# Kernel tuning notes

Measured on AMD Instinct MI355X. Metric: run time of the kernel, lower is better.

## Reference

```python
import jax, jax.numpy as jnp
import numpy as np

H = 32       # total query heads
HK = 8       # kv heads (GQA)
D = 128      # head_dim = hidden // H
HIDDEN = 4096
THETA = 10000.0


def setup_inputs() -> dict:
    key = jax.random.key(0)
    k1, k2, k3 = jax.random.split(key, 3)
    B, S = 2, 2048
    positions = jnp.arange(S, dtype=jnp.int32)
    hidden_states = jax.random.normal(k1, (B, S, HIDDEN), dtype=jnp.float32)
    w_qkv = jax.random.normal(k2, (HIDDEN, (H + 2 * HK) * D), dtype=jnp.float32) * 0.02
    w_o = jax.random.normal(k3, (H * D, HIDDEN), dtype=jnp.float32) * 0.02
    return {"positions": positions, "hidden_states": hidden_states,
            "w_qkv": w_qkv, "w_o": w_o}


def _rope(x, cos, sin):
    # neox-style rotary: split halves, rotate
    x1, x2 = jnp.split(x, 2, axis=-1)
    return jnp.concatenate([x1 * cos - x2 * sin, x2 * cos + x1 * sin], axis=-1)


def reference(positions, hidden_states, w_qkv, w_o):
    B, S, _ = hidden_states.shape
    qkv = hidden_states @ w_qkv                        # [B,S,(H+2HK)*D]
    q, k, v = jnp.split(qkv, [H * D, H * D + HK * D], axis=-1)
    q = q.reshape(B, S, H, D)
    k = k.reshape(B, S, HK, D)
    v = v.reshape(B, S, HK, D)

    inv_freq = 1.0 / (THETA ** (jnp.arange(0, D, 2, dtype=jnp.float32) / D))
    freqs = positions.astype(jnp.float32)[:, None] * inv_freq[None, :]  # [S,D/2]
    cos = jnp.cos(freqs)[None, :, None, :]
    sin = jnp.sin(freqs)[None, :, None, :]
    q = _rope(q, cos, sin)
    k = _rope(k, cos, sin)

    G = H // HK  # query heads per kv head
    qg = q.reshape(B, S, HK, G, D)
    scores = jnp.einsum('bqhgd,bkhd->bhgqk', qg, k) * (D ** -0.5)
    causal = jnp.tril(jnp.ones((S, S), dtype=bool))
    scores = jnp.where(causal[None, None, None], scores, jnp.float32(-1e30))
    probs = jax.nn.softmax(scores, axis=-1)
    out = jnp.einsum('bhgqk,bkhd->bqhgd', probs, v).reshape(B, S, H * D)
    return out @ w_o
```

## Files before the change

kernel.cpp:

```cpp
#include <hip/hip_runtime.h>

typedef unsigned short ushort_t;
typedef __attribute__((ext_vector_type(8))) short short8;
typedef __attribute__((ext_vector_type(4))) unsigned short ushort4_t;
typedef __attribute__((ext_vector_type(4))) float f32x4;

#define NH 32
#define NHK 8
#define HD 128
#define HID 4096
#define NB 2
#define SEQ 2048
#define NQKV ((NH + 2 * NHK) * HD)

static __device__ inline ushort_t f2bu(float x) {
  unsigned u = __builtin_bit_cast(unsigned, x);
  unsigned r = (u + 0x7FFFu + ((u >> 16) & 1u)) >> 16;
  return (ushort_t)r;
}

typedef __attribute__((address_space(1))) void gvoid;
typedef __attribute__((address_space(3))) void lvoid;
static __device__ inline void gld16(const void* g, void* l) {
  __builtin_amdgcn_global_load_lds((gvoid*)g, (lvoid*)l, 16, 0, 0);
}

__global__ void rope_tab_k(const int* __restrict__ positions, float* __restrict__ tab) {
  int i = blockIdx.x * 256 + threadIdx.x;
  int s = i >> 6, d = i & 63;
  float pos = (float)positions[s];
  float f = pos * exp2f(-0.20762050593046014f * (float)d);
  tab[2 * i] = cosf(f);
  tab[2 * i + 1] = sinf(f);
}

__global__ void h2b_k(const float* __restrict__ in, ushort_t* __restrict__ out) {
  long i = ((long)blockIdx.x * 256 + threadIdx.x) * 8;
  f32x4 a = *(const f32x4*)&in[i];
  f32x4 b = *(const f32x4*)&in[i + 4];
  ushort4_t ya, yb;
#pragma unroll
  for (int u = 0; u < 4; ++u) { ya[u] = f2bu(a[u]); yb[u] = f2bu(b[u]); }
  *(ushort4_t*)&out[i] = ya;
  *(ushort4_t*)&out[i + 4] = yb;
}

__global__ void wt_k(const float* __restrict__ in, ushort_t* __restrict__ out,
                     int K, int N) {
  __shared__ ushort_t T[64][72];
  int n0 = blockIdx.x * 64, k0 = blockIdx.y * 64;
  int t = threadIdx.x;
  int kr = t >> 4, nc = (t & 15) * 4;
#pragma unroll
  for (int p = 0; p < 4; ++p) {
    int k = kr + p * 16;
    f32x4 x = *(const f32x4*)&in[(long)(k0 + k) * N + n0 + nc];
    ushort4_t y;
#pragma unroll
    for (int u = 0; u < 4; ++u) y[u] = f2bu(x[u]);
    *(ushort4_t*)&T[k][nc] = y;
  }
  __syncthreads();
  int n = t >> 2, kc = (t & 3) * 16;
  ushort_t tmp[16];
#pragma unroll
  for (int j = 0; j < 16; ++j) tmp[j] = T[kc + j][n];
  *(short8*)&out[(long)(n0 + n) * K + k0 + kc] = *(short8*)&tmp[0];
  *(short8*)&out[(long)(n0 + n) * K + k0 + kc + 8] = *(short8*)&tmp[8];
}

template <int MODE>
__global__ __attribute__((amdgpu_flat_work_group_size(256, 256),
                          amdgpu_waves_per_eu(2, 2)))
void gemm_bt(const ushort_t* __restrict__ A,
             const ushort_t* __restrict__ Bt,
             float* __restrict__ C,
             const float* __restrict__ tab,
             ushort_t* __restrict__ Qo,
             ushort_t* __restrict__ Ko,
             ushort_t* __restrict__ Vo,
             int M, int N, int K) {
  __shared__ ushort_t As[128 * 32];
  __shared__ ushort_t Bs[128 * 32];
  int m0 = blockIdx.y * 128, n0 = blockIdx.x * 128;
  int tid = threadIdx.x;
  int lane = tid & 63, wave = tid >> 6;
  int wm = wave * 32;
  int l15 = lane & 15, quad = lane >> 4;
  f32x4 acc[2][8];
#pragma unroll
  for (int i = 0; i < 2; ++i)
#pragma unroll
    for (int j = 0; j < 8; ++j) acc[i][j] = (f32x4){0.f, 0.f, 0.f, 0.f};

  int iw = wave * 2;
  for (int k0 = 0; k0 < K; k0 += 32) {
    __syncthreads();
#pragma unroll
    for (int ii = 0; ii < 2; ++ii) {
      int i = iw + ii;
      int row = i * 16 + (lane >> 2);
      int gk = ((lane & 3) ^ ((row >> 1) & 3)) * 8;
      gld16(&A[(long)(m0 + row) * K + k0 + gk], &As[i * 512]);
      gld16(&Bt[(long)(n0 + row) * K + k0 + gk], &Bs[i * 512]);
    }
    __syncthreads();
    short8 af[2], bfr[8];
#pragma unroll
    for (int i = 0; i < 2; ++i) {
      int r = wm + i * 16 + l15;
      af[i] = *(short8*)&As[r * 32 + ((quad ^ ((r >> 1) & 3)) << 3)];
    }
#pragma unroll
    for (int j = 0; j < 8; ++j) {
      int r = j * 16 + l15;
      bfr[j] = *(short8*)&Bs[r * 32 + ((quad ^ ((r >> 1) & 3)) << 3)];
    }
#pragma unroll
    for (int i = 0; i < 2; ++i)
#pragma unroll
      for (int j = 0; j < 8; ++j)
        acc[i][j] = __builtin_amdgcn_mfma_f32_16x16x32_bf16(af[i], bfr[j], acc[i][j], 0, 0, 0);
  }

  if (MODE == 0) {
#pragma unroll
    for (int i = 0; i < 2; ++i)
#pragma unroll
      for (int j = 0; j < 8; ++j)
#pragma unroll
        for (int r = 0; r < 4; ++r) {
          int row = m0 + wm + i * 16 + quad * 4 + r;
          int col = n0 + j * 16 + l15;
          C[(long)row * N + col] = acc[i][j][r];
        }
  } else {
    int head = n0 >> 7;
    const float2* tb = (const float2*)tab;
    if (head < NH + NHK) {
      bool isq = head < NH;
      ushort_t* dst = isq ? (Qo + (long)head * SEQ * HD)
                          : (Ko + (long)(head - NH) * SEQ * HD);
      float sc = isq ? 0.08838834764831845f : 1.0f;
#pragma unroll
      for (int i = 0; i < 2; ++i)
#pragma unroll
        for (int r = 0; r < 4; ++r) {
          int s = m0 + wm + i * 16 + quad * 4 + r;
#pragma unroll
          for (int j = 0; j < 4; ++j) {
            int d = j * 16 + l15;
            float2 cs = tb[s * 64 + d];
            float x1 = acc[i][j][r], x2 = acc[i][j + 4][r];
            dst[(long)s * HD + d] = f2bu((x1 * cs.x - x2 * cs.y) * sc);
            dst[(long)s * HD + d + 64] = f2bu((x2 * cs.x + x1 * cs.y) * sc);
          }
        }
    } else {
      int hk = head - NH - NHK;
      ushort_t* dst = Vo + (long)hk * HD * SEQ;
#pragma unroll
      for (int i = 0; i < 2; ++i)
#pragma unroll
        for (int j = 0; j < 8; ++j)
#pragma unroll
          for (int r = 0; r < 4; ++r) {
            int s = m0 + wm + i * 16 + quad * 4 + r;
            int d = j * 16 + l15;
            dst[(long)d * SEQ + s] = f2bu(acc[i][j][r]);
          }
    }
  }
}

template <int MODE, typename TA>
__global__ __attribute__((amdgpu_flat_work_group_size(256, 256),
                          amdgpu_waves_per_eu(2, 2)))
void gemm_kn(const TA* __restrict__ A,
             const float* __restrict__ B,
             float* __restrict__ C,
             const float* __restrict__ tab,
             ushort_t* __restrict__ Qo,
             ushort_t* __restrict__ Ko,
             ushort_t* __restrict__ Vo,
             int M, int N, int K) {
  __shared__ ushort_t As[128][40];
  __shared__ ushort_t Bs[128 * 32];
  int m0 = blockIdx.y * 128, n0 = blockIdx.x * 128;
  int tid = threadIdx.x;
  int lane = tid & 63, wave = tid >> 6;
  int wm = wave * 32;
  int l15 = lane & 15, quad = lane >> 4;
  f32x4 acc[2][8];
#pragma unroll
  for (int i = 0; i < 2; ++i)
#pragma unroll
    for (int j = 0; j < 8; ++j) acc[i][j] = (f32x4){0.f, 0.f, 0.f, 0.f};

  for (int k0 = 0; k0 < K; k0 += 32) {
    __syncthreads();
    if constexpr (sizeof(TA) == 2) {
#pragma unroll
      for (int it = 0; it < 2; ++it) {
        int v = tid + it * 256;
        int row = v >> 2, kc = (v & 3) * 8;
        *(short8*)&As[row][kc] =
            *(const short8*)&A[(long)(m0 + row) * K + k0 + kc];
      }
    } else {
#pragma unroll
      for (int it = 0; it < 4; ++it) {
        int v = tid + it * 256;
        int row = v >> 3, kc = (v & 7) * 4;
        f32x4 x = *(const f32x4*)&A[(long)(m0 + row) * K + k0 + kc];
        ushort4_t y;
#pragma unroll
        for (int u = 0; u < 4; ++u) y[u] = f2bu(x[u]);
        *(ushort4_t*)&As[row][kc] = y;
      }
    }
#pragma unroll
    for (int it = 0; it < 4; ++it) {
      int v = tid + it * 256;
      int kr = v >> 5, nc = (v & 31) * 4;
      f32x4 x = *(const f32x4*)&B[(long)(k0 + kr) * N + n0 + nc];
      int kg = (kr >> 3) << 3, ke = kr & 7;
#pragma unroll
      for (int u = 0; u < 4; ++u) {
        int n = nc + u;
        Bs[n * 32 + ((kg ^ (((n >> 2) & 3) << 3))) + ke] = f2bu(x[u]);
      }
    }
    __syncthreads();
    short8 af[2], bfr[8];
#pragma unroll
    for (int i = 0; i < 2; ++i) af[i] = *(short8*)&As[wm + i * 16 + l15][quad * 8];
#pragma unroll
    for (int j = 0; j < 8; ++j) {
      int n = j * 16 + l15;
      bfr[j] = *(short8*)&Bs[n * 32 + ((quad ^ ((n >> 2) & 3)) << 3)];
    }
#pragma unroll
    for (int i = 0; i < 2; ++i)
#pragma unroll
      for (int j = 0; j < 8; ++j)
        acc[i][j] = __builtin_amdgcn_mfma_f32_16x16x32_bf16(af[i], bfr[j], acc[i][j], 0, 0, 0);
  }

  if (MODE == 0) {
#pragma unroll
    for (int i = 0; i < 2; ++i)
#pragma unroll
      for (int j = 0; j < 8; ++j)
#pragma unroll
        for (int r = 0; r < 4; ++r) {
          int row = m0 + wm + i * 16 + quad * 4 + r;
          int col = n0 + j * 16 + l15;
          C[(long)row * N + col] = acc[i][j][r];
        }
  } else {
    int head = n0 >> 7;
    const float2* tb = (const float2*)tab;
    if (head < NH + NHK) {
      bool isq = head < NH;
      ushort_t* dst = isq ? (Qo + (long)head * SEQ * HD)
                          : (Ko + (long)(head - NH) * SEQ * HD);
      float sc = isq ? 0.08838834764831845f : 1.0f;
#pragma unroll
      for (int i = 0; i < 2; ++i)
#pragma unroll
        for (int r = 0; r < 4; ++r) {
          int s = m0 + wm + i * 16 + quad * 4 + r;
#pragma unroll
          for (int j = 0; j < 4; ++j) {
            int d = j * 16 + l15;
            float2 cs = tb[s * 64 + d];
            float x1 = acc[i][j][r], x2 = acc[i][j + 4][r];
            dst[(long)s * HD + d] = f2bu((x1 * cs.x - x2 * cs.y) * sc);
            dst[(long)s * HD + d + 64] = f2bu((x2 * cs.x + x1 * cs.y) * sc);
          }
        }
    } else {
      int hk = head - NH - NHK;
      ushort_t* dst = Vo + (long)hk * HD * SEQ;
#pragma unroll
      for (int i = 0; i < 2; ++i)
#pragma unroll
        for (int j = 0; j < 8; ++j)
#pragma unroll
          for (int r = 0; r < 4; ++r) {
            int s = m0 + wm + i * 16 + quad * 4 + r;
            int d = j * 16 + l15;
            dst[(long)d * SEQ + s] = f2bu(acc[i][j][r]);
          }
    }
  }
}

__global__ __launch_bounds__(256, 2) void attn_k(const ushort_t* __restrict__ Q,
                                                 const ushort_t* __restrict__ Kg,
                                                 const ushort_t* __restrict__ Vt,
                                                 ushort_t* __restrict__ Aout) {
  __shared__ ushort_t Ks[64][136];
  __shared__ ushort_t Vs[128][72];
  __shared__ ushort_t Ps[4][16][72];
  int qt = ((int)gridDim.x - 1 - blockIdx.x) * 64;
  int h = blockIdx.y;
  int hk = h >> 2;
  const ushort_t* Qh = Q + (long)h * SEQ * HD;
  const ushort_t* Kh = Kg + (long)hk * SEQ * HD;
  const ushort_t* Vh = Vt + (long)hk * HD * SEQ;
  int tid = threadIdx.x, lane = tid & 63, wave = tid >> 6;
  int l15 = lane & 15, quad = lane >> 4;
  int qw = qt + wave * 16;
  short8 qf[4];
#pragma unroll
  for (int c = 0; c < 4; ++c)
    qf[c] = *(const short8*)&Qh[(long)(qw + l15) * HD + c * 32 + quad * 8];
  f32x4 O[8];
#pragma unroll
  for (int dt = 0; dt < 8; ++dt) O[dt] = (f32x4){0.f, 0.f, 0.f, 0.f};
  float mrow[4], lrow[4];
#pragma unroll
  for (int r = 0; r < 4; ++r) { mrow[r] = -1e30f; lrow[r] = 0.f; }
  int kend = qt + 64;
  for (int kc = 0; kc < kend; kc += 64) {
    __syncthreads();
#pragma unroll
    for (int i = 0; i < 4; ++i) {
      int v = tid + i * 256;
      int kr = v >> 4, dc = (v & 15) * 8;
      *(short8*)&Ks[kr][dc] = *(const short8*)&Kh[(long)(kc + kr) * HD + dc];
    }
#pragma unroll
    for (int i = 0; i < 4; ++i) {
      int v = tid + i * 256;
      int dr = v >> 3, kcol = (v & 7) * 8;
      *(short8*)&Vs[dr][kcol] = *(const short8*)&Vh[(long)dr * SEQ + kc + kcol];
    }
    __syncthreads();
    bool active = (kc <= qw + 15);
    if (active) {
      f32x4 S[4];
#pragma unroll
      for (int t = 0; t < 4; ++t) S[t] = (f32x4){0.f, 0.f, 0.f, 0.f};
#pragma unroll
      for (int c = 0; c < 4; ++c) {
#pragma unroll
        for (int t = 0; t < 4; ++t) {
          short8 kf = *(short8*)&Ks[t * 16 + l15][c * 32 + quad * 8];
          S[t] = __builtin_amdgcn_mfma_f32_16x16x32_bf16(qf[c], kf, S[t], 0, 0, 0);
        }
      }
#pragma unroll
      for (int r = 0; r < 4; ++r) {
        int qrow = qw + quad * 4 + r;
        float vv[4];
#pragma unroll
        for (int t = 0; t < 4; ++t)
          vv[t] = (kc + t * 16 + l15 <= qrow) ? S[t][r] : -1e30f;
        float mx = fmaxf(fmaxf(vv[0], vv[1]), fmaxf(vv[2], vv[3]));
        mx = fmaxf(mx, __shfl_xor(mx, 1, 64));
        mx = fmaxf(mx, __shfl_xor(mx, 2, 64));
        mx = fmaxf(mx, __shfl_xor(mx, 4, 64));
        mx = fmaxf(mx, __shfl_xor(mx, 8, 64));
        float mnew = fmaxf(mrow[r], mx);
        float alpha = __expf(mrow[r] - mnew);
        float p[4];
#pragma unroll
        for (int t = 0; t < 4; ++t) p[t] = __expf(vv[t] - mnew);
        float rs = (p[0] + p[1]) + (p[2] + p[3]);
        rs += __shfl_xor(rs, 1, 64);
        rs += __shfl_xor(rs, 2, 64);
        rs += __shfl_xor(rs, 4, 64);
        rs += __shfl_xor(rs, 8, 64);
        lrow[r] = lrow[r] * alpha + rs;
        mrow[r] = mnew;
#pragma unroll
        for (int dt = 0; dt < 8; ++dt) O[dt][r] *= alpha;
#pragma unroll
        for (int t = 0; t < 4; ++t)
          Ps[wave][quad * 4 + r][t * 16 + l15] = f2bu(p[t]);
      }
    }
    __syncthreads();
    if (active) {
      short8 pf0 = *(short8*)&Ps[wave][l15][quad * 8];
      short8 pf1 = *(short8*)&Ps[wave][l15][32 + quad * 8];
#pragma unroll
      for (int dt = 0; dt < 8; ++dt) {
        short8 vf0 = *(short8*)&Vs[dt * 16 + l15][quad * 8];
        short8 vf1 = *(short8*)&Vs[dt * 16 + l15][32 + quad * 8];
        O[dt] = __builtin_amdgcn_mfma_f32_16x16x32_bf16(pf0, vf0, O[dt], 0, 0, 0);
        O[dt] = __builtin_amdgcn_mfma_f32_16x16x32_bf16(pf1, vf1, O[dt], 0, 0, 0);
      }
    }
  }
#pragma unroll
  for (int dt = 0; dt < 8; ++dt)
#pragma unroll
    for (int r = 0; r < 4; ++r) {
      int q = qw + quad * 4 + r;
      float o = O[dt][r] / lrow[r];
      Aout[(long)q * (NH * HD) + h * HD + dt * 16 + l15] = f2bu(o);
    }
}

extern "C" void kernel_launch(void* const* d_in, const int* in_sizes, int n_in,
                              void* d_out, int out_size, void* d_ws, size_t ws_size,
                              hipStream_t stream) {
  const int* positions = (const int*)d_in[0];
  const float* hidden = (const float*)d_in[1];
  const float* w_qkv = (const float*)d_in[2];
  const float* w_o = (const float*)d_in[3];
  char* ws = (char*)d_ws;
  ushort_t* Qb = (ushort_t*)(ws + 0L);
  ushort_t* Kb = (ushort_t*)(ws + 16777216L);
  ushort_t* Vtb = (ushort_t*)(ws + 20971520L);
  ushort_t* attno = (ushort_t*)(ws + 25165824L);
  float* tab = (float*)attno;
  ushort_t* hb16 = (ushort_t*)(ws + 41943040L);
  ushort_t* wqkvT = (ushort_t*)(ws + 75497472L);
  ushort_t* woT = (ushort_t*)(ws + 125829120L);
  float* outf = (float*)d_out;
  bool big = ws_size >= 159383552ULL;

  if (big) {
    h2b_k<<<dim3((NB * SEQ * HID) / (256 * 8)), 256, 0, stream>>>(hidden, hb16);
    wt_k<<<dim3(NQKV / 64, HID / 64), 256, 0, stream>>>(w_qkv, wqkvT, HID, NQKV);
    wt_k<<<dim3(HID / 64, HID / 64), 256, 0, stream>>>(w_o, woT, HID, HID);
  }
  for (int b = 0; b < NB; ++b) {
    rope_tab_k<<<dim3((SEQ * 64) / 256), 256, 0, stream>>>(positions, tab);
    if (big) {
      gemm_bt<1><<<dim3(NQKV / 128, SEQ / 128), 256, 0, stream>>>(
          hb16 + (long)b * SEQ * HID, wqkvT, nullptr, tab, Qb, Kb, Vtb,
          SEQ, NQKV, HID);
    } else {
      gemm_kn<1, float><<<dim3(NQKV / 128, SEQ / 128), 256, 0, stream>>>(
          hidden + (long)b * SEQ * HID, w_qkv, nullptr, tab, Qb, Kb, Vtb,
          SEQ, NQKV, HID);
    }
    attn_k<<<dim3(SEQ / 64, NH), 256, 0, stream>>>(Qb, Kb, Vtb, attno);
    if (big) {
      gemm_bt<0><<<dim3(HID / 128, SEQ / 128), 256, 0, stream>>>(
          attno, woT, outf + (long)b * SEQ * HID, nullptr, nullptr, nullptr,
          nullptr, SEQ, HID, HID);
    } else {
      gemm_kn<0, ushort_t><<<dim3(HID / 128, SEQ / 128), 256, 0, stream>>>(
          attno, w_o, outf + (long)b * SEQ * HID, nullptr, nullptr, nullptr,
          nullptr, SEQ, HID, HID);
    }
  }
}
```

Baseline: 1.158 ms.

## Double-buffer LDS tiles in bf16 GEMM to overlap global loads with MFMA

Splits the shared-memory A and B tiles of the GEMM into two buffers. The next K-slice is prefetched with global_load_lds into the idle buffer while MFMAs run on the current one, leaving one barrier per iteration instead of two. This is meant to hide global memory latency behind compute. It doubles LDS use per block, which could lower occupancy, though waves_per_eu is already fixed at 2.

Result: no change. 1.158 ms (+0.0%).

```diff
diff --git a/kernel.cpp b/kernel.cpp
--- a/kernel.cpp
+++ b/kernel.cpp
@@ -80,8 +80,8 @@
              ushort_t* __restrict__ Ko,
              ushort_t* __restrict__ Vo,
              int M, int N, int K) {
-  __shared__ ushort_t As[128 * 32];
-  __shared__ ushort_t Bs[128 * 32];
+  __shared__ ushort_t As[2][128 * 32];
+  __shared__ ushort_t Bs[2][128 * 32];
   int m0 = blockIdx.y * 128, n0 = blockIdx.x * 128;
   int tid = threadIdx.x;
   int lane = tid & 63, wave = tid >> 6;
@@ -94,34 +94,45 @@
     for (int j = 0; j < 8; ++j) acc[i][j] = (f32x4){0.f, 0.f, 0.f, 0.f};
 
   int iw = wave * 2;
-  for (int k0 = 0; k0 < K; k0 += 32) {
-    __syncthreads();
-#pragma unroll
-    for (int ii = 0; ii < 2; ++ii) {
-      int i = iw + ii;
-      int row = i * 16 + (lane >> 2);
-      int gk = ((lane & 3) ^ ((row >> 1) & 3)) * 8;
-      gld16(&A[(long)(m0 + row) * K + k0 + gk], &As[i * 512]);
-      gld16(&Bt[(long)(n0 + row) * K + k0 + gk], &Bs[i * 512]);
-    }
-    __syncthreads();
+  int r0 = iw * 16 + (lane >> 2);
+  int gk0 = ((lane & 3) ^ ((r0 >> 1) & 3)) * 8;
+  int r1 = r0 + 16;
+  int gk1 = ((lane & 3) ^ ((r1 >> 1) & 3)) * 8;
+
+#define STAGE(buf, k0)                                                   \
+  do {                                                                   \
+    gld16(&A[(long)(m0 + r0) * K + (k0) + gk0], &As[buf][iw * 512]);     \
+    gld16(&Bt[(long)(n0 + r0) * K + (k0) + gk0], &Bs[buf][iw * 512]);    \
+    gld16(&A[(long)(m0 + r1) * K + (k0) + gk1], &As[buf][iw * 512 + 512]); \
+    gld16(&Bt[(long)(n0 + r1) * K + (k0) + gk1], &Bs[buf][iw * 512 + 512]); \
+  } while (0)
+
+  int NT = K >> 5;
+  STAGE(0, 0);
+  __syncthreads();
+  int cur = 0;
+  for (int t = 0; t < NT; ++t) {
+    if (t + 1 < NT) STAGE(cur ^ 1, (t + 1) << 5);
     short8 af[2], bfr[8];
 #pragma unroll
     for (int i = 0; i < 2; ++i) {
       int r = wm + i * 16 + l15;
-      af[i] = *(short8*)&As[r * 32 + ((quad ^ ((r >> 1) & 3)) << 3)];
+      af[i] = *(short8*)&As[cur][r * 32 + ((quad ^ ((r >> 1) & 3)) << 3)];
     }
 #pragma unroll
     for (int j = 0; j < 8; ++j) {
       int r = j * 16 + l15;
-      bfr[j] = *(short8*)&Bs[r * 32 + ((quad ^ ((r >> 1) & 3)) << 3)];
+      bfr[j] = *(short8*)&Bs[cur][r * 32 + ((quad ^ ((r >> 1) & 3)) << 3)];
     }
 #pragma unroll
     for (int i = 0; i < 2; ++i)
 #pragma unroll
       for (int j = 0; j < 8; ++j)
         acc[i][j] = __builtin_amdgcn_mfma_f32_16x16x32_bf16(af[i], bfr[j], acc[i][j], 0, 0, 0);
-  }
+    __syncthreads();
+    cur ^= 1;
+  }
+#undef STAGE
 
   if (MODE == 0) {
 #pragma unroll
```
